# Performance work log

Measured on AMD Instinct MI355X. Metric: run time of the kernel, lower is better.

Reference implementation:

```python
import jax, jax.numpy as jnp
import numpy as np

B, S, D = 8, 2048, 1024
D_FF = 1024  # FeedForward default d_ff
EPS = 1e-5   # nn.LayerNorm default


def layernorm(x, g, b):
    mu = jnp.mean(x, axis=-1, keepdims=True)
    var = jnp.mean(jnp.square(x - mu), axis=-1, keepdims=True)
    return (x - mu) * jax.lax.rsqrt(var + EPS) * g + b


def setup_inputs() -> dict:
    key = jax.random.key(0)
    ks = jax.random.split(key, 12)
    s = 1.0 / np.sqrt(D)
    return {
        "x": jax.random.normal(ks[0], (B, S, D), jnp.float32),
        "mask": jax.random.randint(ks[1], (B, S), 0, 2, jnp.int32),
        "ln1_g": jnp.ones((D,), jnp.float32),
        "ln1_b": jnp.zeros((D,), jnp.float32),
        "Wq": jax.random.normal(ks[2], (D, D), jnp.float32) * s,
        "bq": jnp.zeros((D,), jnp.float32),
        "Wk": jax.random.normal(ks[3], (D, D), jnp.float32) * s,
        "bk": jnp.zeros((D,), jnp.float32),
        "Wo": jax.random.normal(ks[4], (D, D), jnp.float32) * s,
        "bo": jnp.zeros((D,), jnp.float32),
        "ln2_g": jnp.ones((D,), jnp.float32),
        "ln2_b": jnp.zeros((D,), jnp.float32),
        "W1": jax.random.normal(ks[5], (D, D_FF), jnp.float32) * s,
        "b1": jnp.zeros((D_FF,), jnp.float32),
        "W2": jax.random.normal(ks[6], (D_FF, D), jnp.float32) * (1.0 / np.sqrt(D_FF)),
        "b2": jnp.zeros((D,), jnp.float32),
    }


def reference(x, mask, ln1_g, ln1_b, Wq, bq, Wk, bk, Wo, bo, ln2_g, ln2_b, W1, b1, W2, b2):
    # pre-norm
    xn = layernorm(x, ln1_g, ln1_b)
    q = xn @ Wq + bq
    k = xn @ Wk + bk
    v = xn @ Wk + bk  # faithful bug: original uses k_linear for v
    scores = jnp.einsum('bqd,bkd->bqk', q, k) / np.sqrt(D)
    scores = jnp.where(mask[:, None, :] == 0, jnp.float32(-1e9), scores)
    w = jax.nn.softmax(scores, axis=-1)
    attn = jnp.einsum('bqk,bkd->bqd', w, v) @ Wo + bo
    x2 = x + attn  # dropout identity (eval)
    xn2 = layernorm(x2, ln2_g, ln2_b)
    ff = jax.nn.relu(xn2 @ W1 + b1) @ W2 + b2
    out = x2 + ff
    return (out, w)
```

## Files before the change

kernel.cpp:

```cpp
#include <hip/hip_runtime.h>
#include <cstdint>
#include <cstddef>

#define BB 8
#define SS 2048
#define DD 1024

typedef unsigned short bf16_t;
typedef __attribute__((ext_vector_type(8))) short bf16x8;
typedef __attribute__((ext_vector_type(4))) float f32x4;
typedef __attribute__((ext_vector_type(4))) short short4v;

#define EPI_BF16   0
#define EPI_SCORES 1
#define EPI_RESID  2

__device__ __forceinline__ bf16_t f2bf(float f) {
  union { float f; unsigned u; } v; v.f = f;
  unsigned r = v.u + 0x7FFFu + ((v.u >> 16) & 1u);
  return (bf16_t)(r >> 16);
}

__device__ __forceinline__ void async_copy16(const void* g, void* l) {
  auto gp = reinterpret_cast<unsigned int __attribute__((address_space(1)))*>(
      reinterpret_cast<uintptr_t>(g));
  auto lp = reinterpret_cast<unsigned int __attribute__((address_space(3)))*>(
      reinterpret_cast<uintptr_t>(l));
  __builtin_amdgcn_global_load_lds(gp, lp, 16, 0, 0);
}

struct GemmP {
  const bf16_t* __restrict__ A;
  const bf16_t* __restrict__ BT;
  void*         __restrict__ C;
  const float*  __restrict__ bias;
  const float*  __restrict__ bias2;
  const float*  __restrict__ resid;
  const int*    __restrict__ mask;
  int Mt, Nt, Z, nchunk;
  int K, lda, ldb, ldc;
  long long sA, sB, sC, sMask;
  float scale;
};

#define MM(i, j, Af, Bf) \
  acc[i][j] = __builtin_amdgcn_mfma_f32_16x16x32_bf16(Af, Bf, acc[i][j], 0, 0, 0)

#define LDA8(D, MH)                                                        \
  { const char* Ah_ = ldsc + (D) * 65536 + (MH) * 16384;                   \
    aF[0] = *(const bf16x8*)(Ah_ + aro +    0 + s0);                       \
    aF[1] = *(const bf16x8*)(Ah_ + aro + 2048 + s0);                       \
    aF[2] = *(const bf16x8*)(Ah_ + aro + 4096 + s0);                       \
    aF[3] = *(const bf16x8*)(Ah_ + aro + 6144 + s0);                       \
    aF[4] = *(const bf16x8*)(Ah_ + aro +    0 + s1);                       \
    aF[5] = *(const bf16x8*)(Ah_ + aro + 2048 + s1);                       \
    aF[6] = *(const bf16x8*)(Ah_ + aro + 4096 + s1);                       \
    aF[7] = *(const bf16x8*)(Ah_ + aro + 6144 + s1); }

#define LDB4(D, NH, BF)                                                    \
  { const char* Bh_ = ldsc + (D) * 65536 + 32768 + (NH) * 16384;           \
    BF[0] = *(const bf16x8*)(Bh_ + bro +    0 + s0);                       \
    BF[1] = *(const bf16x8*)(Bh_ + bro + 2048 + s0);                       \
    BF[2] = *(const bf16x8*)(Bh_ + bro +    0 + s1);                       \
    BF[3] = *(const bf16x8*)(Bh_ + bro + 2048 + s1); }

#define MFMA16(MH, NH, BF)                                                 \
  __builtin_amdgcn_s_setprio(1);                                           \
  MM((MH)*4+0,(NH)*2+0,aF[0],BF[0]); MM((MH)*4+1,(NH)*2+0,aF[1],BF[0]);    \
  MM((MH)*4+2,(NH)*2+0,aF[2],BF[0]); MM((MH)*4+3,(NH)*2+0,aF[3],BF[0]);    \
  MM((MH)*4+0,(NH)*2+1,aF[0],BF[1]); MM((MH)*4+1,(NH)*2+1,aF[1],BF[1]);    \
  MM((MH)*4+2,(NH)*2+1,aF[2],BF[1]); MM((MH)*4+3,(NH)*2+1,aF[3],BF[1]);    \
  MM((MH)*4+0,(NH)*2+0,aF[4],BF[2]); MM((MH)*4+1,(NH)*2+0,aF[5],BF[2]);    \
  MM((MH)*4+2,(NH)*2+0,aF[6],BF[2]); MM((MH)*4+3,(NH)*2+0,aF[7],BF[2]);    \
  MM((MH)*4+0,(NH)*2+1,aF[4],BF[3]); MM((MH)*4+1,(NH)*2+1,aF[5],BF[3]);    \
  MM((MH)*4+2,(NH)*2+1,aF[6],BF[3]); MM((MH)*4+3,(NH)*2+1,aF[7],BF[3]);    \
  __builtin_amdgcn_s_setprio(0);

template <int EPI, bool RELU>
__device__ __forceinline__ void gemm_core(const GemmP p, int b, char* ldsc)
{
  const int Cchunk = (p.Z * p.Mt * p.Nt) >> 3;
  int idx = (b & 7) * Cchunk + (b >> 3);
  const int per_z = p.Mt * p.Nt;
  const int z = idx / per_z;  idx -= z * per_z;
  const int per_nc = p.Mt * p.nchunk;
  const int nc = idx / per_nc; idx -= nc * per_nc;
  const int mt = idx / p.nchunk;
  const int nin = idx - mt * p.nchunk;
  const int m0 = mt * 256;
  const int n0 = (nc * p.nchunk + nin) * 256;

  const int tid  = threadIdx.x;
  const int wave = tid >> 6;
  const int lane = tid & 63;
  const int wr   = wave >> 2, wc = wave & 3;
  const int lr   = lane & 15, quad = lane >> 4;

  const bf16_t* Ab = p.A  + (size_t)z * (size_t)p.sA;
  const bf16_t* Bb = p.BT + (size_t)z * (size_t)p.sB;

  f32x4 acc[8][4];
#pragma unroll
  for (int i = 0; i < 8; ++i)
#pragma unroll
    for (int j = 0; j < 4; ++j)
#pragma unroll
      for (int r = 0; r < 4; ++r) acc[i][j][r] = 0.0f;

  const bf16_t* gA[2]; const bf16_t* gB[2]; char* lA[2]; char* lB[2];
#pragma unroll
  for (int u = 0; u < 2; ++u) {
    const int c = tid + u * 512;
    const int rl = c >> 3;
    const int csw = (((c & 7) ^ (rl & 7)) << 3);
    const int rowA = ((rl & 64) << 1) + (rl & 63);
    const int rowB = ((rl & 96) << 1) + (rl & 31);
    gA[u] = Ab + (size_t)(m0 + rowA) * p.lda + csw;
    gB[u] = Bb + (size_t)(n0 + rowB) * p.ldb + csw;
    lA[u] = ldsc + c * 16;
    lB[u] = ldsc + 32768 + c * 16;
  }
  const int ldA64 = p.lda << 6, ldB64 = p.ldb << 5;

  auto stageA = [&](int d, int mh, int kt) {
    const int go = mh * ldA64 + kt;
    const int lo = d * 65536 + mh * 16384;
#pragma unroll
    for (int u = 0; u < 2; ++u) async_copy16(gA[u] + go, lA[u] + lo);
  };
  auto stageB = [&](int d, int nh, int kt) {
    const int go = nh * ldB64 + kt;
    const int lo = d * 65536 + nh * 16384;
#pragma unroll
    for (int u = 0; u < 2; ++u) async_copy16(gB[u] + go, lB[u] + lo);
  };

  const int s0  = ((quad ^ (lr & 7)) << 4);
  const int s1  = s0 ^ 64;
  const int aro = (wr * 64 + lr) << 7;
  const int bro = (wc * 32 + lr) << 7;

  bf16x8 aF[8];
  bf16x8 bF0[4], bF1[4];

  const int NT = p.K >> 6;

  stageA(0, 0, 0); stageA(0, 1, 0); stageB(0, 0, 0); stageB(0, 1, 0);
  if (NT > 1) {
    stageA(1, 0, 64); stageB(1, 0, 64);
    asm volatile("s_waitcnt vmcnt(4)" ::: "memory");
  } else {
    asm volatile("s_waitcnt vmcnt(0)" ::: "memory");
  }
  __builtin_amdgcn_s_barrier();

#pragma unroll 2
  for (int t = 0; t < NT; ++t) {
    const int d  = t & 1;
    const int k1 = (t + 1) << 6;
    const int k2 = (t + 2) << 6;

    LDA8(d, 0); LDB4(d, 0, bF0);
    if (t + 1 < NT) stageA(d ^ 1, 1, k1);
    __builtin_amdgcn_s_barrier();
    MFMA16(0, 0, bF0);

    LDB4(d, 1, bF1);
    if (t + 1 < NT) stageB(d ^ 1, 1, k1);
    __builtin_amdgcn_s_barrier();
    MFMA16(0, 1, bF1);

    LDA8(d, 1);
    if (t + 2 < NT) stageA(d, 0, k2);
    __builtin_amdgcn_s_barrier();
    MFMA16(1, 1, bF1);

    if (t + 2 < NT) {
      stageB(d, 0, k2);
      asm volatile("s_waitcnt vmcnt(4)" ::: "memory");
    } else {
      asm volatile("s_waitcnt vmcnt(0)" ::: "memory");
    }
    __builtin_amdgcn_s_barrier();
    MFMA16(1, 0, bF0);
  }

  if constexpr (EPI == EPI_BF16) {
    char* Wb = ldsc + wave * 16384;
#pragma unroll
    for (int i = 0; i < 8; ++i) {
      const int mb = (i >> 2) * 64 + (i & 3) * 16 + quad * 4;
#pragma unroll
      for (int j = 0; j < 4; ++j) {
        const int nl = (j >> 1) * 32 + (j & 1) * 16 + lr;
        const int gn = n0 + wc * 64 + nl;
        const float bv = (p.bias2 && gn >= 1024) ? p.bias2[gn - 1024]
                       : (p.bias ? p.bias[gn] : 0.0f);
#pragma unroll
        for (int r = 0; r < 4; ++r) {
          float v = acc[i][j][r] + bv;
          if (RELU) v = fmaxf(v, 0.0f);
          const int m = mb + r;
          const int nb = nl * 2;
          const int phys = (m << 7) + (((nb & ~15) ^ ((m & 7) << 4)) | (nb & 15));
          *(bf16_t*)(Wb + phys) = f2bf(v);
        }
      }
    }
    asm volatile("s_waitcnt lgkmcnt(0)" ::: "memory");
    bf16_t* Cb = (bf16_t*)p.C + (size_t)z * (size_t)p.sC
               + (size_t)(m0 + wr * 128) * p.ldc + (n0 + wc * 64);
#pragma unroll
    for (int q = 0; q < 16; ++q) {
      const int m = q * 8 + (lane >> 3);
      const int c = lane & 7;
      const bf16x8 vv = *(const bf16x8*)(Wb + (m << 7) + (((c ^ (m & 7)) << 4)));
      *(bf16x8*)(Cb + (size_t)m * p.ldc + c * 8) = vv;
    }
  } else {
    char* Wb = ldsc + wave * 16384;
#pragma unroll
    for (int hh = 0; hh < 2; ++hh) {
#pragma unroll
      for (int ii = 0; ii < 4; ++ii) {
        const int i = hh * 4 + ii;
        const int ml = ii * 16 + quad * 4;
#pragma unroll
        for (int j = 0; j < 4; ++j) {
          const int nl = (j >> 1) * 32 + (j & 1) * 16 + lr;
          const int gn = n0 + wc * 64 + nl;
          float addv = 0.0f; int mk = 1;
          if constexpr (EPI == EPI_RESID) addv = p.bias ? p.bias[gn] : 0.0f;
          if constexpr (EPI == EPI_SCORES)
            mk = p.mask[(size_t)z * (size_t)p.sMask + gn];
#pragma unroll
          for (int r = 0; r < 4; ++r) {
            const int m = ml + r;
            float v = acc[i][j][r];
            if constexpr (EPI == EPI_SCORES) v = mk ? v * p.scale : -1e9f;
            else v += addv;
            const int nph = nl ^ (((m >> 2) & 3) << 2);
            *(float*)(Wb + m * 256 + nph * 4) = v;
          }
        }
      }
      asm volatile("s_waitcnt lgkmcnt(0)" ::: "memory");
      const int mb = m0 + wr * 128 + hh * 64;
      const int gn0 = n0 + wc * 64 + lr * 4;
#pragma unroll
      for (int q = 0; q < 16; ++q) {
        const int m = q * 4 + quad;
        const int nph = (lr * 4) ^ (((m >> 2) & 3) << 2);
        f32x4 v = *(const f32x4*)(Wb + m * 256 + nph * 4);
        const size_t off = (size_t)z * (size_t)p.sC
                         + (size_t)(mb + m) * p.ldc + gn0;
        if constexpr (EPI == EPI_RESID) {
          const f32x4 rv = *(const f32x4*)(p.resid + off);
          v = v + rv;
        }
        *(f32x4*)((float*)p.C + off) = v;
      }
      if (hh == 0) { asm volatile("s_waitcnt lgkmcnt(0)" ::: "memory"); }
    }
  }
}

template <int EPI, bool RELU>
__global__ __launch_bounds__(512, 2)
void gemm256(GemmP p)
{
  __shared__ __align__(16) char lds_[131072];
  gemm_core<EPI, RELU>(p, blockIdx.x, lds_);
}

__global__ __launch_bounds__(512, 2)
void gemm_pair(GemmP p1, int n1, GemmP p2)
{
  __shared__ __align__(16) char lds_[131072];
  if ((int)blockIdx.x < n1) gemm_core<EPI_SCORES, false>(p1, blockIdx.x, lds_);
  else                      gemm_core<EPI_BF16,   false>(p2, blockIdx.x - n1, lds_);
}

__device__ __forceinline__ void ln_body(const float* __restrict__ x,
                                        const float* __restrict__ g,
                                        const float* __restrict__ b,
                                        bf16_t* __restrict__ out,
                                        int row, int t, float* red)
{
  const int wave = t >> 6, lane = t & 63;
  const float4 v = ((const float4*)(x + (size_t)row * DD))[t];

  float s = v.x + v.y + v.z + v.w;
#pragma unroll
  for (int o = 32; o > 0; o >>= 1) s += __shfl_down(s, o);
  if (lane == 0) red[wave] = s;
  __syncthreads();
  const float mu = (red[0] + red[1] + red[2] + red[3]) * (1.0f / DD);

  const float d0 = v.x - mu, d1 = v.y - mu, d2 = v.z - mu, d3 = v.w - mu;
  float ss = d0 * d0 + d1 * d1 + d2 * d2 + d3 * d3;
#pragma unroll
  for (int o = 32; o > 0; o >>= 1) ss += __shfl_down(ss, o);
  if (lane == 0) red[4 + wave] = ss;
  __syncthreads();
  const float var = (red[4] + red[5] + red[6] + red[7]) * (1.0f / DD);
  const float rs  = rsqrtf(var + 1e-5f);

  const float4 gg = ((const float4*)g)[t];
  const float4 bb = ((const float4*)b)[t];
  short4v o;
  o.x = (short)f2bf(d0 * rs * gg.x + bb.x);
  o.y = (short)f2bf(d1 * rs * gg.y + bb.y);
  o.z = (short)f2bf(d2 * rs * gg.z + bb.z);
  o.w = (short)f2bf(d3 * rs * gg.w + bb.w);
  *(short4v*)(out + (size_t)row * DD + t * 4) = o;
}

__global__ __launch_bounds__(256)
void softmax_kernel(float* __restrict__ w, bf16_t* __restrict__ wb)
{
  __shared__ float red[8];
  const size_t rowoff = (size_t)blockIdx.x * SS;
  float* p = w + rowoff;
  const int t = threadIdx.x;
  const int wave = t >> 6, lane = t & 63;
  float4 v0 = ((float4*)p)[t];
  float4 v1 = ((float4*)p)[t + 256];

  float m = fmaxf(fmaxf(fmaxf(v0.x, v0.y), fmaxf(v0.z, v0.w)),
                  fmaxf(fmaxf(v1.x, v1.y), fmaxf(v1.z, v1.w)));
#pragma unroll
  for (int o = 32; o > 0; o >>= 1) m = fmaxf(m, __shfl_down(m, o));
  if (lane == 0) red[wave] = m;
  __syncthreads();
  m = fmaxf(fmaxf(red[0], red[1]), fmaxf(red[2], red[3]));

  v0.x = __expf(v0.x - m); v0.y = __expf(v0.y - m);
  v0.z = __expf(v0.z - m); v0.w = __expf(v0.w - m);
  v1.x = __expf(v1.x - m); v1.y = __expf(v1.y - m);
  v1.z = __expf(v1.z - m); v1.w = __expf(v1.w - m);

  float s = v0.x + v0.y + v0.z + v0.w + v1.x + v1.y + v1.z + v1.w;
#pragma unroll
  for (int o = 32; o > 0; o >>= 1) s += __shfl_down(s, o);
  if (lane == 0) red[4 + wave] = s;
  __syncthreads();
  const float inv = 1.0f / (red[4] + red[5] + red[6] + red[7]);

  v0.x *= inv; v0.y *= inv; v0.z *= inv; v0.w *= inv;
  v1.x *= inv; v1.y *= inv; v1.z *= inv; v1.w *= inv;
  ((float4*)p)[t] = v0;
  ((float4*)p)[t + 256] = v1;

  short4v o0 = { (short)f2bf(v0.x), (short)f2bf(v0.y), (short)f2bf(v0.z), (short)f2bf(v0.w) };
  short4v o1 = { (short)f2bf(v1.x), (short)f2bf(v1.y), (short)f2bf(v1.z), (short)f2bf(v1.w) };
  *(short4v*)(wb + rowoff + t * 4)         = o0;
  *(short4v*)(wb + rowoff + (t + 256) * 4) = o1;
}

template <typename ST>
__device__ __forceinline__ void transpose_body(const ST* __restrict__ in,
                                               bf16_t* __restrict__ out,
                                               int R, int ldin,
                                               long long inB, long long outB,
                                               int xb, int yb, int zb,
                                               int tx, int ty, float* tile)
{
  const size_t zi = (size_t)zb * (size_t)inB;
  const size_t zo = (size_t)zb * (size_t)outB;
  const int c0 = xb * 32, r0 = yb * 32;
#pragma unroll
  for (int k = 0; k < 32; k += 8) {
    ST raw = in[zi + (size_t)(r0 + ty + k) * ldin + (c0 + tx)];
    float v;
    if constexpr (sizeof(ST) == 2) {
      v = __uint_as_float(((unsigned)(unsigned short)raw) << 16);
    } else {
      v = (float)raw;
    }
    tile[(ty + k) * 33 + tx] = v;
  }
  __syncthreads();
#pragma unroll
  for (int k = 0; k < 32; k += 8)
    out[zo + (size_t)(c0 + ty + k) * R + (r0 + tx)] = f2bf(tile[tx * 33 + ty + k]);
}

__global__ __launch_bounds__(256)
void prep_kernel(const float* __restrict__ Wq, const float* __restrict__ Wk,
                 const float* __restrict__ Wo, const float* __restrict__ W1,
                 const float* __restrict__ W2,
                 bf16_t* __restrict__ WqkT, bf16_t* __restrict__ WoT,
                 bf16_t* __restrict__ W1T, bf16_t* __restrict__ W2T,
                 const float* __restrict__ x, const float* __restrict__ g,
                 const float* __restrict__ b, bf16_t* __restrict__ xn)
{
  __shared__ float smem[32 * 33];
  const int bid = blockIdx.x;
  const int tid = threadIdx.x;
  if (bid < 5120) {
    const int wi = bid >> 10;
    const int rem = bid & 1023;
    const float* src = wi == 0 ? Wq : wi == 1 ? Wk : wi == 2 ? Wo : wi == 3 ? W1 : W2;
    bf16_t* dst = wi == 0 ? WqkT : wi == 1 ? (WqkT + (size_t)DD * DD)
                 : wi == 2 ? WoT : wi == 3 ? W1T : W2T;
    transpose_body<float>(src, dst, DD, DD, 0, 0,
                          rem & 31, rem >> 5, 0, tid & 31, tid >> 5, smem);
  } else {
    ln_body(x, g, b, xn, bid - 5120, tid, smem);
  }
}

__global__ __launch_bounds__(256)
void ln_kernel(const float* __restrict__ x, const float* __restrict__ g,
               const float* __restrict__ b, bf16_t* __restrict__ out)
{
  __shared__ float red[8];
  ln_body(x, g, b, out, blockIdx.x, threadIdx.x, red);
}

extern "C" void kernel_launch(void* const* d_in, const int* in_sizes, int n_in,
                              void* d_out, int out_size, void* d_ws, size_t ws_size,
                              hipStream_t stream)
{
  const float* x    = (const float*)d_in[0];
  const int*   mask = (const int*)d_in[1];
  const float* ln1g = (const float*)d_in[2];
  const float* ln1b = (const float*)d_in[3];
  const float* Wq   = (const float*)d_in[4];
  const float* bq   = (const float*)d_in[5];
  const float* Wk   = (const float*)d_in[6];
  const float* bk   = (const float*)d_in[7];
  const float* Wo   = (const float*)d_in[8];
  const float* bo   = (const float*)d_in[9];
  const float* ln2g = (const float*)d_in[10];
  const float* ln2b = (const float*)d_in[11];
  const float* W1   = (const float*)d_in[12];
  const float* b1   = (const float*)d_in[13];
  const float* W2   = (const float*)d_in[14];
  const float* b2   = (const float*)d_in[15];

  float* out  = (float*)d_out;
  float* wout = out + (size_t)BB * SS * DD;

  char* ws = (char*)d_ws;
  size_t off = 0;
  auto alloc = [&](size_t bytes) {
    char* p = ws + off; off += (bytes + 255) & ~(size_t)255; return p;
  };
  bf16_t* WqkT = (bf16_t*)alloc((size_t)2 * DD * DD * 2);
  bf16_t* WoT  = (bf16_t*)alloc((size_t)DD * DD * 2);
  bf16_t* W1T  = (bf16_t*)alloc((size_t)DD * DD * 2);
  bf16_t* W2T  = (bf16_t*)alloc((size_t)DD * DD * 2);
  bf16_t* QKb  = (bf16_t*)alloc((size_t)BB * SS * 2 * DD * 2);
  char*   Rwb  = alloc((size_t)64 * 1024 * 1024);
  bf16_t* KWoT = (bf16_t*)alloc((size_t)BB * SS * DD * 2);

  bf16_t* wbf = (bf16_t*)Rwb;
  bf16_t* xn2 = (bf16_t*)Rwb;
  bf16_t* h   = (bf16_t*)(Rwb + (size_t)32 * 1024 * 1024);

  bf16_t* xn = (bf16_t*)wout;
  float*  x2 = out;

  const dim3 tb(256);
  const dim3 tg(512);
  const long long SD   = (long long)SS * DD;
  const long long S2   = (long long)SS * SS;
  const long long QKs  = (long long)SS * 2 * DD;

  prep_kernel<<<dim3(5120 + BB * SS), tb, 0, stream>>>(
      Wq, Wk, Wo, W1, W2, WqkT, WoT, W1T, W2T, x, ln1g, ln1b, xn);

  gemm256<EPI_BF16, false><<<dim3(512), tg, 0, stream>>>(GemmP{
      xn, WqkT, QKb, bq, bk, nullptr, nullptr,
      64, 8, 1, 8, DD, DD, DD, 2 * DD, 0, 0, 0, 0, 1.0f});

  {
    GemmP ps{QKb, QKb + DD, wout, nullptr, nullptr, nullptr, mask,
             8, 8, BB, 8, DD, 2 * DD, 2 * DD, SS, QKs, QKs, S2, SS, 0.03125f};
    GemmP pk{WoT, QKb + DD, KWoT, nullptr, nullptr, nullptr, nullptr,
             4, 8, BB, 8, DD, DD, 2 * DD, SS, 0, QKs, SD, 0, 1.0f};
    gemm_pair<<<dim3(768), tg, 0, stream>>>(ps, 512, pk);
  }

  softmax_kernel<<<dim3(BB * SS), tb, 0, stream>>>(wout, wbf);

  gemm256<EPI_RESID, false><<<dim3(256), tg, 0, stream>>>(GemmP{
      wbf, KWoT, x2, bo, nullptr, x, nullptr,
      8, 4, BB, 4, SS, SS, SS, DD, S2, SD, SD, 0, 1.0f});

  ln_kernel<<<dim3(BB * SS), tb, 0, stream>>>(x2, ln2g, ln2b, xn2);

  gemm256<EPI_BF16, true><<<dim3(256), tg, 0, stream>>>(GemmP{
      xn2, W1T, h, b1, nullptr, nullptr, nullptr,
      64, 4, 1, 4, DD, DD, DD, DD, 0, 0, 0, 0, 1.0f});

  gemm256<EPI_RESID, false><<<dim3(256), tg, 0, stream>>>(GemmP{
      h, W2T, out, b2, nullptr, x2, nullptr,
      64, 4, 1, 4, DD, DD, DD, DD, 0, 0, 0, 0, 1.0f});
}
```

Before: 681.8 us.

## Fuse all stages into one persistent kernel with grid-wide barriers

Replaces the eight separate launches (prep, QK GEMM, scores+KWo pair, softmax, attention GEMM, LN2, FF1, FF2) with a single persistent 256-block kernel that loops over the work items of each stage and separates stages with an atomic-counter grid barrier. Layernorm and softmax are rewritten for 512-thread blocks, and the GEMM epilogues gain a trailing barrier so shared memory can be reused safely. The intent is to remove launch gaps and tail effects between kernels. In exchange, the elementwise stages now run on only 256 blocks, each grid barrier spins on a global atomic, and the GEMM stages that previously launched 512 or 768 blocks are serialized across loop iterations.

After: 1.343 ms. 97.0% more time.

```diff
diff --git a/kernel.cpp b/kernel.cpp
--- a/kernel.cpp
+++ b/kernel.cpp
@@ -9,7 +9,6 @@
 typedef unsigned short bf16_t;
 typedef __attribute__((ext_vector_type(8))) short bf16x8;
 typedef __attribute__((ext_vector_type(4))) float f32x4;
-typedef __attribute__((ext_vector_type(4))) short short4v;
 
 #define EPI_BF16   0
 #define EPI_SCORES 1
@@ -30,13 +29,13 @@
 }
 
 struct GemmP {
-  const bf16_t* __restrict__ A;
-  const bf16_t* __restrict__ BT;
-  void*         __restrict__ C;
-  const float*  __restrict__ bias;
-  const float*  __restrict__ bias2;
-  const float*  __restrict__ resid;
-  const int*    __restrict__ mask;
+  const bf16_t* A;
+  const bf16_t* BT;
+  void*         C;
+  const float*  bias;
+  const float*  bias2;
+  const float*  resid;
+  const int*    mask;
   int Mt, Nt, Z, nchunk;
   int K, lda, ldb, ldc;
   long long sA, sB, sC, sMask;
@@ -217,6 +216,7 @@
       const bf16x8 vv = *(const bf16x8*)(Wb + (m << 7) + (((c ^ (m & 7)) << 4)));
       *(bf16x8*)(Cb + (size_t)m * p.ldc + c * 8) = vv;
     }
+    __builtin_amdgcn_s_barrier();
   } else {
     char* Wb = ldsc + wave * 16384;
 #pragma unroll
@@ -262,161 +262,155 @@
       }
       if (hh == 0) { asm volatile("s_waitcnt lgkmcnt(0)" ::: "memory"); }
     }
-  }
-}
-
-template <int EPI, bool RELU>
-__global__ __launch_bounds__(512, 2)
-void gemm256(GemmP p)
-{
-  __shared__ __align__(16) char lds_[131072];
-  gemm_core<EPI, RELU>(p, blockIdx.x, lds_);
-}
-
-__global__ __launch_bounds__(512, 2)
-void gemm_pair(GemmP p1, int n1, GemmP p2)
-{
-  __shared__ __align__(16) char lds_[131072];
-  if ((int)blockIdx.x < n1) gemm_core<EPI_SCORES, false>(p1, blockIdx.x, lds_);
-  else                      gemm_core<EPI_BF16,   false>(p2, blockIdx.x - n1, lds_);
-}
-
-__device__ __forceinline__ void ln_body(const float* __restrict__ x,
-                                        const float* __restrict__ g,
-                                        const float* __restrict__ b,
-                                        bf16_t* __restrict__ out,
-                                        int row, int t, float* red)
+    __builtin_amdgcn_s_barrier();
+  }
+}
+
+__device__ __forceinline__ void ln512(const float* __restrict__ x,
+                                      const float* __restrict__ g,
+                                      const float* __restrict__ b,
+                                      bf16_t* __restrict__ out,
+                                      int row, int t, float* red)
 {
   const int wave = t >> 6, lane = t & 63;
-  const float4 v = ((const float4*)(x + (size_t)row * DD))[t];
-
-  float s = v.x + v.y + v.z + v.w;
+  const float2 v = ((const float2*)(x + (size_t)row * DD))[t];
+  float s = v.x + v.y;
 #pragma unroll
   for (int o = 32; o > 0; o >>= 1) s += __shfl_down(s, o);
   if (lane == 0) red[wave] = s;
   __syncthreads();
-  const float mu = (red[0] + red[1] + red[2] + red[3]) * (1.0f / DD);
-
-  const float d0 = v.x - mu, d1 = v.y - mu, d2 = v.z - mu, d3 = v.w - mu;
-  float ss = d0 * d0 + d1 * d1 + d2 * d2 + d3 * d3;
+  const float mu = (red[0]+red[1]+red[2]+red[3]+red[4]+red[5]+red[6]+red[7]) * (1.0f/DD);
+  const float d0 = v.x - mu, d1 = v.y - mu;
+  float ss = d0*d0 + d1*d1;
 #pragma unroll
   for (int o = 32; o > 0; o >>= 1) ss += __shfl_down(ss, o);
-  if (lane == 0) red[4 + wave] = ss;
-  __syncthreads();
-  const float var = (red[4] + red[5] + red[6] + red[7]) * (1.0f / DD);
-  const float rs  = rsqrtf(var + 1e-5f);
-
-  const float4 gg = ((const float4*)g)[t];
-  const float4 bb = ((const float4*)b)[t];
-  short4v o;
-  o.x = (short)f2bf(d0 * rs * gg.x + bb.x);
-  o.y = (short)f2bf(d1 * rs * gg.y + bb.y);
-  o.z = (short)f2bf(d2 * rs * gg.z + bb.z);
-  o.w = (short)f2bf(d3 * rs * gg.w + bb.w);
-  *(short4v*)(out + (size_t)row * DD + t * 4) = o;
-}
-
-__global__ __launch_bounds__(256)
-void softmax_kernel(float* __restrict__ w, bf16_t* __restrict__ wb)
-{
-  __shared__ float red[8];
-  const size_t rowoff = (size_t)blockIdx.x * SS;
-  float* p = w + rowoff;
-  const int t = threadIdx.x;
+  if (lane == 0) red[8+wave] = ss;
+  __syncthreads();
+  const float var = (red[8]+red[9]+red[10]+red[11]+red[12]+red[13]+red[14]+red[15]) * (1.0f/DD);
+  const float rs = rsqrtf(var + 1e-5f);
+  const float2 gg = ((const float2*)g)[t];
+  const float2 bb = ((const float2*)b)[t];
+  const unsigned lo = f2bf(d0*rs*gg.x + bb.x);
+  const unsigned hi = f2bf(d1*rs*gg.y + bb.y);
+  ((unsigned*)(out + (size_t)row * DD))[t] = (hi << 16) | lo;
+  __syncthreads();
+}
+
+__device__ __forceinline__ void softmax512(float* __restrict__ w,
+                                           bf16_t* __restrict__ wb,
+                                           int row, int t, float* red)
+{
+  float* p = w + (size_t)row * SS;
   const int wave = t >> 6, lane = t & 63;
-  float4 v0 = ((float4*)p)[t];
-  float4 v1 = ((float4*)p)[t + 256];
-
-  float m = fmaxf(fmaxf(fmaxf(v0.x, v0.y), fmaxf(v0.z, v0.w)),
-                  fmaxf(fmaxf(v1.x, v1.y), fmaxf(v1.z, v1.w)));
+  float4 v = ((float4*)p)[t];
+  float m = fmaxf(fmaxf(v.x, v.y), fmaxf(v.z, v.w));
 #pragma unroll
   for (int o = 32; o > 0; o >>= 1) m = fmaxf(m, __shfl_down(m, o));
   if (lane == 0) red[wave] = m;
   __syncthreads();
-  m = fmaxf(fmaxf(red[0], red[1]), fmaxf(red[2], red[3]));
-
-  v0.x = __expf(v0.x - m); v0.y = __expf(v0.y - m);
-  v0.z = __expf(v0.z - m); v0.w = __expf(v0.w - m);
-  v1.x = __expf(v1.x - m); v1.y = __expf(v1.y - m);
-  v1.z = __expf(v1.z - m); v1.w = __expf(v1.w - m);
-
-  float s = v0.x + v0.y + v0.z + v0.w + v1.x + v1.y + v1.z + v1.w;
+  m = fmaxf(fmaxf(fmaxf(red[0],red[1]),fmaxf(red[2],red[3])),
+            fmaxf(fmaxf(red[4],red[5]),fmaxf(red[6],red[7])));
+  v.x = __expf(v.x - m); v.y = __expf(v.y - m);
+  v.z = __expf(v.z - m); v.w = __expf(v.w - m);
+  float s = v.x + v.y + v.z + v.w;
 #pragma unroll
   for (int o = 32; o > 0; o >>= 1) s += __shfl_down(s, o);
-  if (lane == 0) red[4 + wave] = s;
-  __syncthreads();
-  const float inv = 1.0f / (red[4] + red[5] + red[6] + red[7]);
-
-  v0.x *= inv; v0.y *= inv; v0.z *= inv; v0.w *= inv;
-  v1.x *= inv; v1.y *= inv; v1.z *= inv; v1.w *= inv;
-  ((float4*)p)[t] = v0;
-  ((float4*)p)[t + 256] = v1;
-
-  short4v o0 = { (short)f2bf(v0.x), (short)f2bf(v0.y), (short)f2bf(v0.z), (short)f2bf(v0.w) };
-  short4v o1 = { (short)f2bf(v1.x), (short)f2bf(v1.y), (short)f2bf(v1.z), (short)f2bf(v1.w) };
-  *(short4v*)(wb + rowoff + t * 4)         = o0;
-  *(short4v*)(wb + rowoff + (t + 256) * 4) = o1;
-}
-
-template <typename ST>
-__device__ __forceinline__ void transpose_body(const ST* __restrict__ in,
+  if (lane == 0) red[8+wave] = s;
+  __syncthreads();
+  const float inv = 1.0f / (red[8]+red[9]+red[10]+red[11]+red[12]+red[13]+red[14]+red[15]);
+  v.x *= inv; v.y *= inv; v.z *= inv; v.w *= inv;
+  ((float4*)p)[t] = v;
+  uint2 u;
+  u.x = ((unsigned)f2bf(v.y) << 16) | (unsigned)f2bf(v.x);
+  u.y = ((unsigned)f2bf(v.w) << 16) | (unsigned)f2bf(v.z);
+  ((uint2*)(wb + (size_t)row * SS))[t] = u;
+  __syncthreads();
+}
+
+__device__ __forceinline__ void transpose_body(const float* __restrict__ in,
                                                bf16_t* __restrict__ out,
-                                               int R, int ldin,
-                                               long long inB, long long outB,
-                                               int xb, int yb, int zb,
+                                               int xb, int yb,
                                                int tx, int ty, float* tile)
 {
-  const size_t zi = (size_t)zb * (size_t)inB;
-  const size_t zo = (size_t)zb * (size_t)outB;
   const int c0 = xb * 32, r0 = yb * 32;
 #pragma unroll
-  for (int k = 0; k < 32; k += 8) {
-    ST raw = in[zi + (size_t)(r0 + ty + k) * ldin + (c0 + tx)];
-    float v;
-    if constexpr (sizeof(ST) == 2) {
-      v = __uint_as_float(((unsigned)(unsigned short)raw) << 16);
-    } else {
-      v = (float)raw;
-    }
-    tile[(ty + k) * 33 + tx] = v;
-  }
-  __syncthreads();
-#pragma unroll
   for (int k = 0; k < 32; k += 8)
-    out[zo + (size_t)(c0 + ty + k) * R + (r0 + tx)] = f2bf(tile[tx * 33 + ty + k]);
-}
-
-__global__ __launch_bounds__(256)
-void prep_kernel(const float* __restrict__ Wq, const float* __restrict__ Wk,
-                 const float* __restrict__ Wo, const float* __restrict__ W1,
-                 const float* __restrict__ W2,
-                 bf16_t* __restrict__ WqkT, bf16_t* __restrict__ WoT,
-                 bf16_t* __restrict__ W1T, bf16_t* __restrict__ W2T,
-                 const float* __restrict__ x, const float* __restrict__ g,
-                 const float* __restrict__ b, bf16_t* __restrict__ xn)
-{
-  __shared__ float smem[32 * 33];
+    tile[(ty + k) * 33 + tx] = in[(size_t)(r0 + ty + k) * DD + (c0 + tx)];
+  __syncthreads();
+#pragma unroll
+  for (int k = 0; k < 32; k += 8)
+    out[(size_t)(c0 + ty + k) * DD + (r0 + tx)] = f2bf(tile[tx * 33 + ty + k]);
+}
+
+__device__ __forceinline__ void gsync(unsigned* bar, unsigned target)
+{
+  __syncthreads();
+  if (threadIdx.x == 0) {
+    __threadfence();
+    __hip_atomic_fetch_add(bar, 1u, __ATOMIC_ACQ_REL, __HIP_MEMORY_SCOPE_AGENT);
+    while (__hip_atomic_load(bar, __ATOMIC_ACQUIRE, __HIP_MEMORY_SCOPE_AGENT) < target)
+      __builtin_amdgcn_s_sleep(2);
+    __threadfence();
+  }
+  __syncthreads();
+}
+
+struct MegaP {
+  const float *Wq, *Wk, *Wo, *W1, *W2;
+  bf16_t *WqkT, *WoT, *W1T, *W2T;
+  const float *x, *ln1g, *ln1b; bf16_t *xn;
+  GemmP qk, sc, kwo, wkwo, ff1, ff2;
+  float *wout; bf16_t *wbf;
+  const float *x2; const float *ln2g, *ln2b; bf16_t *xn2;
+  unsigned* bar;
+};
+
+__global__ __launch_bounds__(512, 2)
+void mega_kernel(MegaP P)
+{
+  __shared__ __align__(16) char lds[131072];
   const int bid = blockIdx.x;
   const int tid = threadIdx.x;
-  if (bid < 5120) {
-    const int wi = bid >> 10;
-    const int rem = bid & 1023;
-    const float* src = wi == 0 ? Wq : wi == 1 ? Wk : wi == 2 ? Wo : wi == 3 ? W1 : W2;
-    bf16_t* dst = wi == 0 ? WqkT : wi == 1 ? (WqkT + (size_t)DD * DD)
-                 : wi == 2 ? WoT : wi == 3 ? W1T : W2T;
-    transpose_body<float>(src, dst, DD, DD, 0, 0,
-                          rem & 31, rem >> 5, 0, tid & 31, tid >> 5, smem);
-  } else {
-    ln_body(x, g, b, xn, bid - 5120, tid, smem);
-  }
-}
-
-__global__ __launch_bounds__(256)
-void ln_kernel(const float* __restrict__ x, const float* __restrict__ g,
-               const float* __restrict__ b, bf16_t* __restrict__ out)
-{
-  __shared__ float red[8];
-  ln_body(x, g, b, out, blockIdx.x, threadIdx.x, red);
+  float* redf = (float*)lds;
+
+  {
+    const int half = tid >> 8, t = tid & 255;
+    float* tile_s = (float*)lds + half * (32 * 33);
+    for (int it = 0; it < 10; ++it) {
+      const int tt = (it * 256 + bid) * 2 + half;
+      const int wi = tt >> 10, rem = tt & 1023;
+      const float* src = wi==0?P.Wq : wi==1?P.Wk : wi==2?P.Wo : wi==3?P.W1 : P.W2;
+      bf16_t* dst = wi==0?P.WqkT : wi==1?(P.WqkT+(size_t)DD*DD)
+                  : wi==2?P.WoT : wi==3?P.W1T : P.W2T;
+      transpose_body(src, dst, rem & 31, rem >> 5, t & 31, t >> 5, tile_s);
+      __syncthreads();
+    }
+    for (int r = bid; r < BB*SS; r += 256) ln512(P.x, P.ln1g, P.ln1b, P.xn, r, tid, redf);
+  }
+  gsync(P.bar, 256);
+
+  for (int i = bid; i < 512; i += 256) gemm_core<EPI_BF16, false>(P.qk, i, lds);
+  gsync(P.bar, 512);
+
+  for (int i = bid; i < 768; i += 256) {
+    if (i < 512) gemm_core<EPI_SCORES, false>(P.sc, i, lds);
+    else         gemm_core<EPI_BF16,   false>(P.kwo, i - 512, lds);
+  }
+  gsync(P.bar, 768);
+
+  for (int r = bid; r < BB*SS; r += 256) softmax512(P.wout, P.wbf, r, tid, redf);
+  gsync(P.bar, 1024);
+
+  gemm_core<EPI_RESID, false>(P.wkwo, bid, lds);
+  gsync(P.bar, 1280);
+
+  for (int r = bid; r < BB*SS; r += 256) ln512(P.x2, P.ln2g, P.ln2b, P.xn2, r, tid, redf);
+  gsync(P.bar, 1536);
+
+  gemm_core<EPI_BF16, true>(P.ff1, bid, lds);
+  gsync(P.bar, 1792);
+
+  gemm_core<EPI_RESID, false>(P.ff2, bid, lds);
 }
 
 extern "C" void kernel_launch(void* const* d_in, const int* in_sizes, int n_in,
@@ -455,6 +449,7 @@
   bf16_t* QKb  = (bf16_t*)alloc((size_t)BB * SS * 2 * DD * 2);
   char*   Rwb  = alloc((size_t)64 * 1024 * 1024);
   bf16_t* KWoT = (bf16_t*)alloc((size_t)BB * SS * DD * 2);
+  unsigned* bar = (unsigned*)alloc(256);
 
   bf16_t* wbf = (bf16_t*)Rwb;
   bf16_t* xn2 = (bf16_t*)Rwb;
@@ -463,40 +458,31 @@
   bf16_t* xn = (bf16_t*)wout;
   float*  x2 = out;
 
-  const dim3 tb(256);
-  const dim3 tg(512);
-  const long long SD   = (long long)SS * DD;
-  const long long S2   = (long long)SS * SS;
-  const long long QKs  = (long long)SS * 2 * DD;
-
-  prep_kernel<<<dim3(5120 + BB * SS), tb, 0, stream>>>(
-      Wq, Wk, Wo, W1, W2, WqkT, WoT, W1T, W2T, x, ln1g, ln1b, xn);
-
-  gemm256<EPI_BF16, false><<<dim3(512), tg, 0, stream>>>(GemmP{
-      xn, WqkT, QKb, bq, bk, nullptr, nullptr,
-      64, 8, 1, 8, DD, DD, DD, 2 * DD, 0, 0, 0, 0, 1.0f});
-
-  {
-    GemmP ps{QKb, QKb + DD, wout, nullptr, nullptr, nullptr, mask,
-             8, 8, BB, 8, DD, 2 * DD, 2 * DD, SS, QKs, QKs, S2, SS, 0.03125f};
-    GemmP pk{WoT, QKb + DD, KWoT, nullptr, nullptr, nullptr, nullptr,
-             4, 8, BB, 8, DD, DD, 2 * DD, SS, 0, QKs, SD, 0, 1.0f};
-    gemm_pair<<<dim3(768), tg, 0, stream>>>(ps, 512, pk);
-  }
-
-  softmax_kernel<<<dim3(BB * SS), tb, 0, stream>>>(wout, wbf);
-
-  gemm256<EPI_RESID, false><<<dim3(256), tg, 0, stream>>>(GemmP{
-      wbf, KWoT, x2, bo, nullptr, x, nullptr,
-      8, 4, BB, 4, SS, SS, SS, DD, S2, SD, SD, 0, 1.0f});
-
-  ln_kernel<<<dim3(BB * SS), tb, 0, stream>>>(x2, ln2g, ln2b, xn2);
-
-  gemm256<EPI_BF16, true><<<dim3(256), tg, 0, stream>>>(GemmP{
-      xn2, W1T, h, b1, nullptr, nullptr, nullptr,
-      64, 4, 1, 4, DD, DD, DD, DD, 0, 0, 0, 0, 1.0f});
-
-  gemm256<EPI_RESID, false><<<dim3(256), tg, 0, stream>>>(GemmP{
-      h, W2T, out, b2, nullptr, x2, nullptr,
-      64, 4, 1, 4, DD, DD, DD, DD, 0, 0, 0, 0, 1.0f});
-}
+  const long long SD  = (long long)SS * DD;
+  const long long S2  = (long long)SS * SS;
+  const long long QKs = (long long)SS * 2 * DD;
+
+  hipMemsetAsync(bar, 0, 256, stream);
+
+  MegaP P;
+  P.Wq = Wq; P.Wk = Wk; P.Wo = Wo; P.W1 = W1; P.W2 = W2;
+  P.WqkT = WqkT; P.WoT = WoT; P.W1T = W1T; P.W2T = W2T;
+  P.x = x; P.ln1g = ln1g; P.ln1b = ln1b; P.xn = xn;
+  P.qk   = GemmP{xn, WqkT, QKb, bq, bk, nullptr, nullptr,
+                 64, 8, 1, 8, DD, DD, DD, 2 * DD, 0, 0, 0, 0, 1.0f};
+  P.sc   = GemmP{QKb, QKb + DD, wout, nullptr, nullptr, nullptr, mask,
+                 8, 8, BB, 8, DD, 2 * DD, 2 * DD, SS, QKs, QKs, S2, SS, 0.03125f};
+  P.kwo  = GemmP{WoT, QKb + DD, KWoT, nullptr, nullptr, nullptr, nullptr,
+                 4, 8, BB, 8, DD, DD, 2 * DD, SS, 0, QKs, SD, 0, 1.0f};
+  P.wkwo = GemmP{wbf, KWoT, x2, bo, nullptr, x, nullptr,
+                 8, 4, BB, 4, SS, SS, SS, DD, S2, SD, SD, 0, 1.0f};
+  P.ff1  = GemmP{xn2, W1T, h, b1, nullptr, nullptr, nullptr,
+                 64, 4, 1, 4, DD, DD, DD, DD, 0, 0, 0, 0, 1.0f};
+  P.ff2  = GemmP{h, W2T, out, b2, nullptr, x2, nullptr,
+                 64, 4, 1, 4, DD, DD, DD, DD, 0, 0, 0, 0, 1.0f};
+  P.wout = wout; P.wbf = wbf;
+  P.x2 = x2; P.ln2g = ln2g; P.ln2b = ln2b; P.xn2 = xn2;
+  P.bar = bar;
+
+  mega_kernel<<<dim3(256), dim3(512), 0, stream>>>(P);
+}
```
